# Kernel tuning notes

Measured on AMD Instinct MI355X. Metric: run time of the kernel, lower is better.

The kernel has to match this reference:

```python
import jax, jax.numpy as jnp
import numpy as np

# Model hyperparameters (from init_kwargs)
D_MODEL, D_STATE, D_CONV, EXPAND, NHEADS, NGROUPS = 1024, 16, 4, 2, 8, 1
D_INNER = D_MODEL * EXPAND                      # 2048
HEADDIM = D_INNER // NHEADS                     # 256
D_XBC = D_INNER + 2 * NGROUPS * D_STATE         # conv channels: x + B + C
D_IN_PROJ = 3 * D_INNER + D_XBC + NHEADS        # z0 + x0 + z(unused) + xBC + dt
BATCH, SEQLEN = 2, 2048
LN_EPS = 1e-5


def setup_inputs() -> dict:
    key = jax.random.key(0)
    ks = jax.random.split(key, 8)
    u = jax.random.normal(ks[0], (BATCH, SEQLEN, D_MODEL), dtype=jnp.float32)
    W_in = jax.random.normal(ks[1], (D_IN_PROJ, D_MODEL), jnp.float32) / np.sqrt(D_MODEL)
    conv_w = jax.random.normal(ks[2], (D_XBC, 1, D_CONV), jnp.float32) / np.sqrt(D_CONV)
    conv_b = jnp.zeros((D_XBC,), jnp.float32)
    # dt_bias = inverse-softplus of dt ~ LogUniform(1e-3, 1e-1), as in source init
    dt = jnp.exp(jax.random.uniform(ks[3], (NHEADS,)) * (np.log(0.1) - np.log(0.001)) + np.log(0.001))
    dt_bias = dt + jnp.log(-jnp.expm1(-dt))
    A_log = jnp.log(jax.random.uniform(ks[4], (NHEADS,), minval=0.9, maxval=0.999))
    D_param = jnp.ones((NHEADS,), jnp.float32)
    ln_gamma = jnp.ones((D_INNER,), jnp.float32)
    ln_beta = jnp.zeros((D_INNER,), jnp.float32)
    W_gate = jax.random.normal(ks[5], (D_INNER, D_INNER), jnp.float32) / np.sqrt(D_INNER)
    b_gate = jnp.zeros((D_INNER,), jnp.float32)
    W_out = jax.random.normal(ks[6], (D_MODEL, 2 * D_INNER), jnp.float32) / np.sqrt(2 * D_INNER)
    return dict(u=u, W_in=W_in, conv_w=conv_w, conv_b=conv_b, dt_bias=dt_bias,
                A_log=A_log, D_param=D_param, ln_gamma=ln_gamma, ln_beta=ln_beta,
                W_gate=W_gate, b_gate=b_gate, W_out=W_out)


def _silu(x):
    return x * jax.nn.sigmoid(x)


def reference(u, W_in, conv_w, conv_b, dt_bias, A_log, D_param,
              ln_gamma, ln_beta, W_gate, b_gate, W_out):
    B, L, _ = u.shape
    zxbcdt = u @ W_in.T                                   # [B,L,D_IN_PROJ]
    z0 = zxbcdt[..., :D_INNER]
    x0 = zxbcdt[..., D_INNER:2 * D_INNER]
    # z = zxbcdt[..., 2*D_INNER:3*D_INNER]  # split but never used in source forward
    xBC = zxbcdt[..., 3 * D_INNER:3 * D_INNER + D_XBC]
    dt = jax.nn.softplus(zxbcdt[..., -NHEADS:] + dt_bias)  # [B,L,H]
    A = -jnp.exp(A_log)                                    # [H], per-head scalar

    # causal depthwise conv1d over time (left pad d_conv-1, crop to L)
    xBC_c = jnp.transpose(xBC, (0, 2, 1))                  # [B,C,L]
    xBC_c = jax.lax.conv_general_dilated(
        xBC_c, conv_w, window_strides=(1,), padding=[(D_CONV - 1, 0)],
        dimension_numbers=('NCH', 'OIH', 'NCH'), feature_group_count=D_XBC)
    xBC = _silu(jnp.transpose(xBC_c, (0, 2, 1)) + conv_b)  # [B,L,C]

    x = xBC[..., :D_INNER].reshape(B, L, NHEADS, HEADDIM)  # [B,L,H,P]
    Bm = xBC[..., D_INNER:D_INNER + D_STATE]               # [B,L,N] (ngroups=1)
    Cm = xBC[..., D_INNER + D_STATE:]                      # [B,L,N]

    def step(h, inp):
        x_t, B_t, C_t, dt_t = inp                          # [B,H,P],[B,N],[B,N],[B,H]
        dA = jnp.exp(dt_t * A)[:, :, None, None]           # [B,H,1,1]
        h = dA * h + (dt_t[:, :, None, None] * x_t[..., None]) * B_t[:, None, None, :]
        y_t = jnp.einsum('bhpn,bn->bhp', h, C_t) + D_param[None, :, None] * x_t
        return h, y_t

    h0 = jnp.zeros((B, NHEADS, HEADDIM, D_STATE), u.dtype)
    xs = (jnp.moveaxis(x, 1, 0), jnp.moveaxis(Bm, 1, 0),
          jnp.moveaxis(Cm, 1, 0), jnp.moveaxis(dt, 1, 0))
    _, y = jax.lax.scan(step, h0, xs)                      # [L,B,H,P]
    y = jnp.moveaxis(y, 0, 1).reshape(B, L, D_INNER)

    # LayerNorm
    mu = y.mean(-1, keepdims=True)
    var = ((y - mu) ** 2).mean(-1, keepdims=True)
    y = (y - mu) * jax.lax.rsqrt(var + LN_EPS) * ln_gamma + ln_beta

    gate = jax.nn.sigmoid(y @ W_gate.T + b_gate)
    y = gate * y

    mlp_skip = _silu(z0) * x0
    return jnp.concatenate([mlp_skip, y], axis=-1) @ W_out.T  # [B,L,D_MODEL]
```

## Files before the change

### kernel.cpp

```cpp
#include <hip/hip_runtime.h>
#include <hip/hip_bf16.h>
#include <math.h>

#define BATCH   2
#define SEQLEN  2048
#define DMODEL  1024
#define DINNER  2048
#define DSTATE  16
#define NHEADS  8
#define HEADDIM 256
#define DXBC    2080
#define NPACK   6184
#define NPAD    6400
#define MROWS   4096
#define CHUNK   64
#define NCHUNK  32
#define BH      16

typedef unsigned int u32;
typedef unsigned short u16;
typedef __attribute__((ext_vector_type(8))) short short8;
typedef __attribute__((ext_vector_type(4))) float f32x4;

#define GLOAD16(g, l) __builtin_amdgcn_global_load_lds( \
    (const __attribute__((address_space(1))) u32*)(g),  \
    (__attribute__((address_space(3))) u32*)(l), 16, 0, 0)

#define MFMA_B16(d, a, b) d = __builtin_amdgcn_mfma_f32_16x16x32_bf16(a, b, d, 0, 0, 0)

__device__ __forceinline__ u16 f2bf(float f) {
  union { float f; u32 u; } v; v.f = f;
  u32 r = v.u + 0x7fff + ((v.u >> 16) & 1);
  return (u16)(r >> 16);
}
__device__ __forceinline__ float bf2f(u16 b) {
  union { u32 u; float f; } v; v.u = ((u32)b) << 16;
  return v.f;
}

struct GParts { float* p0; float* p1; };

#define S_U   1048576
#define S_WG  1048576
#define S_WO  1048576
#define S_WP  1638400
#define S_TOT (S_U + S_WG + S_WO + S_WP)

__global__ void cvt_all(const float* __restrict__ u, const float* __restrict__ Wg,
                        const float* __restrict__ Wo, const float* __restrict__ Win,
                        u16* __restrict__ ub, u16* __restrict__ Wgb,
                        u16* __restrict__ Wob, u16* __restrict__ Wp) {
  for (int i = blockIdx.x * 256 + threadIdx.x; i < S_TOT; i += gridDim.x * 256) {
    const float* src; u16* dst; int idx;
    if (i < S_U) { src = u; dst = ub; idx = i; }
    else if (i < S_U + S_WG) { src = Wg; dst = Wgb; idx = i - S_U; }
    else if (i < S_U + S_WG + S_WO) { src = Wo; dst = Wob; idx = i - S_U - S_WG; }
    else {
      int j = i - S_U - S_WG - S_WO;
      int row = j >> 8, c4 = j & 255;
      ushort4 o = make_ushort4(0, 0, 0, 0);
      if (row < NPACK) {
        int orig = row < 4096 ? row : row + 2048;
        float4 v = ((const float4*)(Win + (size_t)orig * DMODEL))[c4];
        o = make_ushort4(f2bf(v.x), f2bf(v.y), f2bf(v.z), f2bf(v.w));
      }
      ((ushort4*)Wp)[j] = o;
      continue;
    }
    float4 v = ((const float4*)src)[idx];
    ((ushort4*)dst)[idx] = make_ushort4(f2bf(v.x), f2bf(v.y), f2bf(v.z), f2bf(v.w));
  }
}

template <int NL>
__device__ __forceinline__ void stage_rows(const u16* __restrict__ gsrc, int ldk,
                                           char* ldsmat, int row0, int w, int l) {
  const int rl = w * 8 + (l >> 3);
  const int q = ((l & 7) ^ (l >> 3)) * 8;
  #pragma unroll
  for (int j = 0; j < NL; ++j) {
    GLOAD16(gsrc + (size_t)(row0 + j * 64 + rl) * ldk + q,
            ldsmat + (row0 + j * 64 + w * 8) * 128);
  }
}

__device__ __forceinline__ short8 frag8(const char* mat, int row, int q) {
  return *(const short8*)(mat + row * 128 + ((q ^ (row & 7)) << 4));
}

__global__ __launch_bounds__(512, 1) void gemmA(
    const u16* __restrict__ A, const u16* __restrict__ B, int K, int ldk,
    int ldo, u16* __restrict__ outp) {
  __shared__ char lds[131072];
  const int tid = threadIdx.x;
  const int w = tid >> 6, l = tid & 63;
  const int wm = w >> 2, wn = w & 3;
  const int fr = l & 15, g = l >> 4;
  int s = blockIdx.y * gridDim.x + blockIdx.x;
  const int nwg = gridDim.x * gridDim.y;
  s = (s & 7) * (nwg >> 3) + (s >> 3);
  const int bx = s % gridDim.x, by = s / gridDim.x;
  const u16* Ap = A + (size_t)bx * 256 * ldk;
  const u16* Bp = B + (size_t)by * 256 * ldk;
  const int NT = K >> 6;

  f32x4 acc[8][4];
  #pragma unroll
  for (int m = 0; m < 8; ++m)
    #pragma unroll
    for (int n = 0; n < 4; ++n) acc[m][n] = (f32x4){0.f, 0.f, 0.f, 0.f};

  stage_rows<2>(Bp, ldk, lds + 32768, 0, w, l);
  stage_rows<2>(Bp, ldk, lds + 32768, 128, w, l);
  stage_rows<1>(Ap, ldk, lds, 0, w, l);
  stage_rows<1>(Ap, ldk, lds, 128, w, l);
  stage_rows<1>(Ap, ldk, lds, 64, w, l);
  stage_rows<1>(Ap, ldk, lds, 192, w, l);

  for (int t = 0; t < NT; ++t) {
    const bool last = (t == NT - 1);
    const char* cbA = lds + (t & 1) * 65536;
    const char* cbB = cbA + 32768;
    char* nbA = lds + ((t + 1) & 1) * 65536;
    char* nbB = nbA + 32768;
    const u16* An = Ap + (size_t)(t + 1) * 64;
    const u16* Bn = Bp + (size_t)(t + 1) * 64;

    asm volatile("s_waitcnt vmcnt(2)" ::: "memory");
    __builtin_amdgcn_s_barrier();
    __builtin_amdgcn_sched_barrier(0);

    short8 bf0[4], bf1[4];
    #pragma unroll
    for (int n = 0; n < 4; ++n) {
      bf0[n] = frag8(cbB, wn * 64 + n * 16 + fr, g);
      bf1[n] = frag8(cbB, wn * 64 + n * 16 + fr, 4 + g);
    }
    {
      short8 a00 = frag8(cbA, wm * 128 + fr, g);
      short8 a01 = frag8(cbA, wm * 128 + fr, 4 + g);
      short8 a10 = frag8(cbA, wm * 128 + 16 + fr, g);
      short8 a11 = frag8(cbA, wm * 128 + 16 + fr, 4 + g);
      if (!last) stage_rows<2>(Bn, ldk, nbB, 0, w, l);
      asm volatile("s_waitcnt lgkmcnt(0)" ::: "memory");
      __builtin_amdgcn_sched_barrier(0);
      __builtin_amdgcn_s_setprio(1);
      #pragma unroll
      for (int n = 0; n < 4; ++n) { MFMA_B16(acc[0][n], a00, bf0[n]); MFMA_B16(acc[1][n], a10, bf0[n]); }
      #pragma unroll
      for (int n = 0; n < 4; ++n) { MFMA_B16(acc[0][n], a01, bf1[n]); MFMA_B16(acc[1][n], a11, bf1[n]); }
      __builtin_amdgcn_s_setprio(0);
    }
    {
      short8 a00 = frag8(cbA, wm * 128 + 32 + fr, g);
      short8 a01 = frag8(cbA, wm * 128 + 32 + fr, 4 + g);
      short8 a10 = frag8(cbA, wm * 128 + 48 + fr, g);
      short8 a11 = frag8(cbA, wm * 128 + 48 + fr, 4 + g);
      if (!last) stage_rows<2>(Bn, ldk, nbB, 128, w, l);
      asm volatile("s_waitcnt lgkmcnt(0)" ::: "memory");
      __builtin_amdgcn_sched_barrier(0);
      __builtin_amdgcn_s_setprio(1);
      #pragma unroll
      for (int n = 0; n < 4; ++n) { MFMA_B16(acc[2][n], a00, bf0[n]); MFMA_B16(acc[3][n], a10, bf0[n]); }
      #pragma unroll
      for (int n = 0; n < 4; ++n) { MFMA_B16(acc[2][n], a01, bf1[n]); MFMA_B16(acc[3][n], a11, bf1[n]); }
      __builtin_amdgcn_s_setprio(0);
    }
    if (last) { asm volatile("s_waitcnt vmcnt(0)" ::: "memory"); }
    else      { asm volatile("s_waitcnt vmcnt(4)" ::: "memory"); }
    __builtin_amdgcn_s_barrier();
    __builtin_amdgcn_sched_barrier(0);
    {
      short8 a00 = frag8(cbA, wm * 128 + 64 + fr, g);
      short8 a01 = frag8(cbA, wm * 128 + 64 + fr, 4 + g);
      short8 a10 = frag8(cbA, wm * 128 + 80 + fr, g);
      short8 a11 = frag8(cbA, wm * 128 + 80 + fr, 4 + g);
      if (!last) { stage_rows<1>(An, ldk, nbA, 0, w, l); stage_rows<1>(An, ldk, nbA, 128, w, l); }
      asm volatile("s_waitcnt lgkmcnt(0)" ::: "memory");
      __builtin_amdgcn_sched_barrier(0);
      __builtin_amdgcn_s_setprio(1);
      #pragma unroll
      for (int n = 0; n < 4; ++n) { MFMA_B16(acc[4][n], a00, bf0[n]); MFMA_B16(acc[5][n], a10, bf0[n]); }
      #pragma unroll
      for (int n = 0; n < 4; ++n) { MFMA_B16(acc[4][n], a01, bf1[n]); MFMA_B16(acc[5][n], a11, bf1[n]); }
      __builtin_amdgcn_s_setprio(0);
    }
    {
      short8 a00 = frag8(cbA, wm * 128 + 96 + fr, g);
      short8 a01 = frag8(cbA, wm * 128 + 96 + fr, 4 + g);
      short8 a10 = frag8(cbA, wm * 128 + 112 + fr, g);
      short8 a11 = frag8(cbA, wm * 128 + 112 + fr, 4 + g);
      if (!last) { stage_rows<1>(An, ldk, nbA, 64, w, l); stage_rows<1>(An, ldk, nbA, 192, w, l); }
      asm volatile("s_waitcnt lgkmcnt(0)" ::: "memory");
      __builtin_amdgcn_sched_barrier(0);
      __builtin_amdgcn_s_setprio(1);
      #pragma unroll
      for (int n = 0; n < 4; ++n) { MFMA_B16(acc[6][n], a00, bf0[n]); MFMA_B16(acc[7][n], a10, bf0[n]); }
      #pragma unroll
      for (int n = 0; n < 4; ++n) { MFMA_B16(acc[6][n], a01, bf1[n]); MFMA_B16(acc[7][n], a11, bf1[n]); }
      __builtin_amdgcn_s_setprio(0);
    }
  }

  const int er = g * 4;
  #pragma unroll
  for (int m = 0; m < 8; ++m)
    #pragma unroll
    for (int n = 0; n < 4; ++n)
      #pragma unroll
      for (int j = 0; j < 4; ++j) {
        int row = bx * 256 + wm * 128 + m * 16 + er + j;
        int col = by * 256 + wn * 64 + n * 16 + fr;
        outp[(size_t)row * ldo + col] = f2bf(acc[m][n][j]);
      }
}

template <int EPI>
__global__ __launch_bounds__(512, 1) void gemmB(
    const u16* __restrict__ A, const u16* __restrict__ B, int K_loop, int ldk,
    int ldo, void* __restrict__ outp, const float* __restrict__ bias,
    const u16* __restrict__ gate_in, GParts gp) {
  __shared__ char lds[3 * 49152];
  const int tid = threadIdx.x;
  const int w = tid >> 6, l = tid & 63;
  const int wm = w >> 1, wn = w & 1;
  const int fr = l & 15, g = l >> 4;
  int s = blockIdx.y * gridDim.x + blockIdx.x;
  const int nwg = gridDim.x * gridDim.y;
  s = (s & 7) * (nwg >> 3) + (s >> 3);
  const int bx = s % gridDim.x, by = s / gridDim.x;
  const u16* Ap = A + (size_t)bx * 256 * ldk + (size_t)blockIdx.z * K_loop;
  const u16* Bp = B + (size_t)by * 128 * ldk + (size_t)blockIdx.z * K_loop;
  const int NT = K_loop >> 6;

  f32x4 acc[4][4];
  #pragma unroll
  for (int m = 0; m < 4; ++m)
    #pragma unroll
    for (int n = 0; n < 4; ++n) acc[m][n] = (f32x4){0.f, 0.f, 0.f, 0.f};

  #pragma unroll
  for (int p = 0; p < 2; ++p) {
    char* bA = lds + p * 49152;
    char* bB = bA + 32768;
    const u16* Ak = Ap + (size_t)p * 64;
    const u16* Bk = Bp + (size_t)p * 64;
    stage_rows<1>(Bk, ldk, bB, 0, w, l);
    stage_rows<1>(Bk, ldk, bB, 64, w, l);
    stage_rows<1>(Ak, ldk, bA, 0, w, l);
    stage_rows<1>(Ak, ldk, bA, 64, w, l);
    stage_rows<1>(Ak, ldk, bA, 128, w, l);
    stage_rows<1>(Ak, ldk, bA, 192, w, l);
  }

  int cur = 0;
  for (int t = 0; t < NT; ++t) {
    const bool last = (t == NT - 1);
    const bool dostage = (t + 2 < NT);
    int st = cur + 2; if (st >= 3) st -= 3;
    const char* cbA = lds + cur * 49152;
    const char* cbB = cbA + 32768;
    char* nbA = lds + st * 49152;
    char* nbB = nbA + 32768;
    const u16* An = Ap + (size_t)(t + 2) * 64;
    const u16* Bn = Bp + (size_t)(t + 2) * 64;

    if (last) { asm volatile("s_waitcnt vmcnt(0)" ::: "memory"); }
    else      { asm volatile("s_waitcnt vmcnt(6)" ::: "memory"); }
    __builtin_amdgcn_s_barrier();
    __builtin_amdgcn_sched_barrier(0);

    short8 bf0[4], bf1[4];
    #pragma unroll
    for (int n = 0; n < 4; ++n) {
      bf0[n] = frag8(cbB, wn * 64 + n * 16 + fr, g);
      bf1[n] = frag8(cbB, wn * 64 + n * 16 + fr, 4 + g);
    }
    {
      short8 a00 = frag8(cbA, wm * 64 + fr, g);
      short8 a01 = frag8(cbA, wm * 64 + fr, 4 + g);
      short8 a10 = frag8(cbA, wm * 64 + 16 + fr, g);
      short8 a11 = frag8(cbA, wm * 64 + 16 + fr, 4 + g);
      if (dostage) {
        stage_rows<1>(Bn, ldk, nbB, 0, w, l);
        stage_rows<1>(Bn, ldk, nbB, 64, w, l);
        stage_rows<1>(An, ldk, nbA, 0, w, l);
      }
      asm volatile("s_waitcnt lgkmcnt(0)" ::: "memory");
      __builtin_amdgcn_sched_barrier(0);
      __builtin_amdgcn_s_setprio(1);
      #pragma unroll
      for (int n = 0; n < 4; ++n) { MFMA_B16(acc[0][n], a00, bf0[n]); MFMA_B16(acc[1][n], a10, bf0[n]); }
      #pragma unroll
      for (int n = 0; n < 4; ++n) { MFMA_B16(acc[0][n], a01, bf1[n]); MFMA_B16(acc[1][n], a11, bf1[n]); }
      __builtin_amdgcn_s_setprio(0);
    }
    {
      short8 a00 = frag8(cbA, wm * 64 + 32 + fr, g);
      short8 a01 = frag8(cbA, wm * 64 + 32 + fr, 4 + g);
      short8 a10 = frag8(cbA, wm * 64 + 48 + fr, g);
      short8 a11 = frag8(cbA, wm * 64 + 48 + fr, 4 + g);
      if (dostage) {
        stage_rows<1>(An, ldk, nbA, 64, w, l);
        stage_rows<1>(An, ldk, nbA, 128, w, l);
        stage_rows<1>(An, ldk, nbA, 192, w, l);
      }
      asm volatile("s_waitcnt lgkmcnt(0)" ::: "memory");
      __builtin_amdgcn_sched_barrier(0);
      __builtin_amdgcn_s_setprio(1);
      #pragma unroll
      for (int n = 0; n < 4; ++n) { MFMA_B16(acc[2][n], a00, bf0[n]); MFMA_B16(acc[3][n], a10, bf0[n]); }
      #pragma unroll
      for (int n = 0; n < 4; ++n) { MFMA_B16(acc[2][n], a01, bf1[n]); MFMA_B16(acc[3][n], a11, bf1[n]); }
      __builtin_amdgcn_s_setprio(0);
    }
    cur = cur + 1; if (cur >= 3) cur = 0;
  }

  const int er = g * 4;
  float* pp = nullptr;
  if (EPI == 2) pp = blockIdx.z == 0 ? gp.p0 : gp.p1;
  #pragma unroll
  for (int m = 0; m < 4; ++m)
    #pragma unroll
    for (int n = 0; n < 4; ++n)
      #pragma unroll
      for (int j = 0; j < 4; ++j) {
        int row = bx * 256 + wm * 64 + m * 16 + er + j;
        int col = by * 128 + wn * 64 + n * 16 + fr;
        float v = acc[m][n][j];
        if (EPI == 1) {
          float gt = 1.f / (1.f + __expf(-(v + bias[col])));
          float nv = bf2f(gate_in[(size_t)row * 2048 + col]);
          ((u16*)outp)[(size_t)row * 4096 + 2048 + col] = f2bf(gt * nv);
        } else {
          pp[(size_t)row * ldo + col] = v;
        }
      }
}

__global__ void reduce2(const float* __restrict__ p0, const float* __restrict__ p1,
                        float* __restrict__ out) {
  const int n4 = MROWS * DMODEL / 4;
  for (int i = blockIdx.x * 256 + threadIdx.x; i < n4; i += gridDim.x * 256) {
    float4 a = ((const float4*)p0)[i];
    float4 b = ((const float4*)p1)[i];
    float4 o;
    o.x = a.x + b.x; o.y = a.y + b.y; o.z = a.z + b.z; o.w = a.w + b.w;
    ((float4*)out)[i] = o;
  }
}

#define NB_CONV 33280
#define NB_MLP  8192
#define NB_DT   128

__global__ void prep_kernel(const u16* __restrict__ zx, const float* __restrict__ cw,
                            const float* __restrict__ cb, u16* __restrict__ xc,
                            float* __restrict__ bc, u16* __restrict__ hcat,
                            const float* __restrict__ dt_bias, float* __restrict__ dtb) {
  int blk = blockIdx.x;
  if (blk < NB_CONV) {
    int idx = blk * 256 + threadIdx.x;
    if (idx >= MROWS * DXBC) return;
    int c = idx % DXBC;
    int m = idx / DXBC;
    int l = m & (SEQLEN - 1);
    float acc = cb[c];
    float w0 = cw[c * 4 + 0], w1 = cw[c * 4 + 1], w2 = cw[c * 4 + 2], w3 = cw[c * 4 + 3];
    const u16* col = zx + (size_t)m * NPAD + 4096 + c;
    acc += w3 * bf2f(col[0]);
    if (l >= 1) acc += w2 * bf2f(col[-NPAD]);
    if (l >= 2) acc += w1 * bf2f(col[-2 * NPAD]);
    if (l >= 3) acc += w0 * bf2f(col[-3 * NPAD]);
    float sv = acc / (1.f + __expf(-acc));
    if (c < DINNER) xc[(size_t)m * DINNER + c] = f2bf(sv);
    else bc[(size_t)m * 32 + (c - DINNER)] = sv;
  } else if (blk < NB_CONV + NB_MLP) {
    int i = (blk - NB_CONV) * 256 + threadIdx.x;
    int m = i >> 9, c4 = (i & 511) * 4;
    const u16* row = zx + (size_t)m * NPAD;
    ushort4 zv = *(const ushort4*)(row + c4);
    ushort4 xv = *(const ushort4*)(row + 2048 + c4);
    float z0, x0;
    ushort4 o;
    z0 = bf2f(zv.x); x0 = bf2f(xv.x); o.x = f2bf(x0 * z0 / (1.f + __expf(-z0)));
    z0 = bf2f(zv.y); x0 = bf2f(xv.y); o.y = f2bf(x0 * z0 / (1.f + __expf(-z0)));
    z0 = bf2f(zv.z); x0 = bf2f(xv.z); o.z = f2bf(x0 * z0 / (1.f + __expf(-z0)));
    z0 = bf2f(zv.w); x0 = bf2f(xv.w); o.w = f2bf(x0 * z0 / (1.f + __expf(-z0)));
    *(ushort4*)(hcat + (size_t)m * 4096 + c4) = o;
  } else {
    int idx = (blk - NB_CONV - NB_MLP) * 256 + threadIdx.x;
    if (idx >= MROWS * NHEADS) return;
    int hd = idx & 7, m = idx >> 3;
    float raw = bf2f(zx[(size_t)m * NPAD + 6176 + hd]) + dt_bias[hd];
    float dtv = raw > 20.f ? raw : log1pf(expf(raw));
    dtb[idx] = dtv;
  }
}

__device__ __forceinline__ int xs_addr(int r, int p) {
  return r * 512 + ((((p >> 3) ^ ((r >> 3) & 3)) & 31) << 4) + (p & 7) * 2;
}
__device__ __forceinline__ int P_addr(int t, int s) {
  return t * 128 + ((((s >> 3) ^ (t & 7)) & 7) << 4) + (s & 7) * 2;
}

__device__ __forceinline__ void stage_x(u16* xs, const u16* __restrict__ xc,
                                        size_t base, int tid) {
  #pragma unroll
  for (int it = 0; it < 8; ++it) {
    int r = it * 8 + (tid >> 5);
    int pc = (tid & 31) * 8;
    short8 v = *(const short8*)(xc + base + (size_t)r * DINNER + pc);
    *(short8*)((char*)xs + xs_addr(r, pc)) = v;
  }
}

__device__ __forceinline__ short8 xfrag(const u16* xs, int k0, int g, int p) {
  short8 v;
  #pragma unroll
  for (int j = 0; j < 8; ++j) {
    int s = k0 + g * 8 + j;
    v[j] = *(const short*)((const char*)xs + xs_addr(s, p));
  }
  return v;
}

__global__ __launch_bounds__(256) void ssd_state(
    const u16* __restrict__ xc, const float* __restrict__ bcb,
    const float* __restrict__ dtb, const float* __restrict__ A_log,
    float* __restrict__ Sbuf, float* __restrict__ lcbuf) {
  __shared__ u16 xs[64 * 256];
  __shared__ float sLC[64], sDT[64];
  __shared__ float wBT[16][65];
  const int tid = threadIdx.x;
  const int bh = blockIdx.x >> 5, c = blockIdx.x & 31;
  const int b = bh >> 3, h = bh & 7;
  const size_t row0 = (size_t)b * SEQLEN + c * CHUNK;
  stage_x(xs, xc, row0 * DINNER + h * HEADDIM, tid);
  if (tid < 64) {
    float dtv = dtb[(row0 + tid) * NHEADS + h];
    float A = -__expf(A_log[h]);
    float s = dtv * A;
    #pragma unroll
    for (int off = 1; off < 64; off <<= 1) {
      float v = __shfl_up(s, off, 64);
      if (tid >= off) s += v;
    }
    sLC[tid] = s; sDT[tid] = dtv;
    lcbuf[(size_t)blockIdx.x * 64 + tid] = s;
  }
  __syncthreads();
  const float lc63 = sLC[63];
  for (int i = tid; i < 1024; i += 256) {
    int n = i & 15, t = i >> 4;
    float w = sDT[t] * __expf(lc63 - sLC[t]);
    wBT[n][t] = w * bcb[(row0 + t) * 32 + n];
  }
  __syncthreads();
  const int lane = tid & 63, w = tid >> 6;
  const int cl = lane & 15, g = lane >> 4;
  f32x4 acc[4];
  #pragma unroll
  for (int pt = 0; pt < 4; ++pt) acc[pt] = (f32x4){0.f, 0.f, 0.f, 0.f};
  #pragma unroll
  for (int kk = 0; kk < 2; ++kk) {
    int k0 = kk * 32;
    short8 af;
    #pragma unroll
    for (int j = 0; j < 8; ++j) af[j] = (short)f2bf(wBT[cl][k0 + g * 8 + j]);
    #pragma unroll
    for (int pt = 0; pt < 4; ++pt) {
      short8 bf = xfrag(xs, k0, g, (w * 4 + pt) * 16 + cl);
      acc[pt] = __builtin_amdgcn_mfma_f32_16x16x32_bf16(af, bf, acc[pt], 0, 0, 0);
    }
  }
  float* Sc = Sbuf + (size_t)blockIdx.x * 16 * 256;
  #pragma unroll
  for (int pt = 0; pt < 4; ++pt)
    #pragma unroll
    for (int j = 0; j < 4; ++j)
      Sc[(g * 4 + j) * 256 + (w * 4 + pt) * 16 + cl] = acc[pt][j];
}

__global__ __launch_bounds__(256) void ssd_combine(
    const float* __restrict__ Sbuf, const float* __restrict__ lcbuf,
    float* __restrict__ Sprev) {
  const int bh = blockIdx.x >> 4, seg = blockIdx.x & 15;
  const int idx = seg * 256 + threadIdx.x;
  float r = 0.f;
  #pragma unroll 1
  for (int c = 0; c < NCHUNK; ++c) {
    size_t o = ((size_t)bh * NCHUNK + c) * 4096 + idx;
    Sprev[o] = r;
    float lam = __expf(lcbuf[((size_t)bh * NCHUNK + c) * 64 + 63]);
    r = lam * r + Sbuf[o];
  }
}

__global__ __launch_bounds__(256) void ssd_out(
    const u16* __restrict__ xc, const float* __restrict__ bcb,
    const float* __restrict__ dtb, const float* __restrict__ lcbuf,
    const float* __restrict__ Sprev, const float* __restrict__ D_par,
    u16* __restrict__ y) {
  __shared__ u16 xs[64 * 256];
  __shared__ u16 P[64 * 64];
  __shared__ u16 sB[64][17], sC[64][17], sCe[64][17];
  __shared__ u16 sSp[256][17];
  __shared__ float sLC[64], sDT[64];
  const int tid = threadIdx.x;
  const int bh = blockIdx.x >> 5, c = blockIdx.x & 31;
  const int b = bh >> 3, h = bh & 7;
  const size_t row0 = (size_t)b * SEQLEN + c * CHUNK;
  stage_x(xs, xc, row0 * DINNER + h * HEADDIM, tid);
  if (tid < 64) {
    sLC[tid] = lcbuf[(size_t)blockIdx.x * 64 + tid];
    sDT[tid] = dtb[(row0 + tid) * NHEADS + h];
  }
  for (int i = tid; i < 1024; i += 256) {
    int n = i & 15, t = i >> 4;
    float Bv = bcb[(row0 + t) * 32 + n];
    float Cv = bcb[(row0 + t) * 32 + 16 + n];
    float e = __expf(lcbuf[(size_t)blockIdx.x * 64 + t]);
    sB[t][n] = f2bf(Bv);
    sC[t][n] = f2bf(Cv);
    sCe[t][n] = f2bf(Cv * e);
  }
  {
    const float* Sp = Sprev + (size_t)blockIdx.x * 4096;
    int p = tid & 255;
    if (tid < 256) {
      #pragma unroll
      for (int n = 0; n < 16; ++n) sSp[p][n] = f2bf(Sp[n * 256 + p]);
    }
  }
  __syncthreads();

  const int lane = tid & 63, w = tid >> 6;
  const int cl = lane & 15, g = lane >> 4;

  f32x4 gacc[4];
  #pragma unroll
  for (int st = 0; st < 4; ++st) gacc[st] = (f32x4){0.f, 0.f, 0.f, 0.f};
  short8 afc = (short8){0, 0, 0, 0, 0, 0, 0, 0};
  if (g < 2) {
    #pragma unroll
    for (int j = 0; j < 8; ++j) afc[j] = (short)sC[w * 16 + cl][g * 8 + j];
  }
  #pragma unroll
  for (int st = 0; st < 4; ++st) {
    short8 bfb = (short8){0, 0, 0, 0, 0, 0, 0, 0};
    if (g < 2) {
      #pragma unroll
      for (int j = 0; j < 8; ++j) bfb[j] = (short)sB[st * 16 + cl][g * 8 + j];
    }
    gacc[st] = __builtin_amdgcn_mfma_f32_16x16x32_bf16(afc, bfb, gacc[st], 0, 0, 0);
  }
  #pragma unroll
  for (int st = 0; st < 4; ++st) {
    #pragma unroll
    for (int j = 0; j < 4; ++j) {
      int t = w * 16 + g * 4 + j;
      int s = st * 16 + cl;
      float v = 0.f;
      if (s <= t) v = gacc[st][j] * sDT[s] * __expf(sLC[t] - sLC[s]);
      *(u16*)((char*)P + P_addr(t, s)) = f2bf(v);
    }
  }
  asm volatile("s_waitcnt lgkmcnt(0)" ::: "memory");
  __builtin_amdgcn_sched_barrier(0);

  f32x4 acc[16];
  #pragma unroll
  for (int pt = 0; pt < 16; ++pt) acc[pt] = (f32x4){0.f, 0.f, 0.f, 0.f};
  #pragma unroll
  for (int kk = 0; kk < 2; ++kk) {
    int k0 = kk * 32;
    short8 ap = *(const short8*)((const char*)P + P_addr(w * 16 + cl, k0 + g * 8));
    #pragma unroll
    for (int pt = 0; pt < 16; ++pt) {
      short8 bf = xfrag(xs, k0, g, pt * 16 + cl);
      acc[pt] = __builtin_amdgcn_mfma_f32_16x16x32_bf16(ap, bf, acc[pt], 0, 0, 0);
    }
  }
  {
    short8 ae = (short8){0, 0, 0, 0, 0, 0, 0, 0};
    if (g < 2) {
      #pragma unroll
      for (int j = 0; j < 8; ++j) ae[j] = (short)sCe[w * 16 + cl][g * 8 + j];
    }
    #pragma unroll
    for (int pt = 0; pt < 16; ++pt) {
      short8 bs = (short8){0, 0, 0, 0, 0, 0, 0, 0};
      if (g < 2) {
        #pragma unroll
        for (int j = 0; j < 8; ++j) bs[j] = (short)sSp[pt * 16 + cl][g * 8 + j];
      }
      acc[pt] = __builtin_amdgcn_mfma_f32_16x16x32_bf16(ae, bs, acc[pt], 0, 0, 0);
    }
  }
  const float Dv = D_par[h];
  #pragma unroll
  for (int pt = 0; pt < 16; ++pt) {
    #pragma unroll
    for (int j = 0; j < 4; ++j) {
      int t = w * 16 + g * 4 + j;
      int p = pt * 16 + cl;
      float xv = bf2f(*(const u16*)((const char*)xs + xs_addr(t, p)));
      float v = acc[pt][j] + Dv * xv;
      y[(row0 + t) * DINNER + h * HEADDIM + p] = f2bf(v);
    }
  }
}

__global__ __launch_bounds__(256) void ln_kernel(const u16* __restrict__ y,
                                                 const float* __restrict__ gamma,
                                                 const float* __restrict__ beta,
                                                 u16* __restrict__ nrm) {
  const int row = blockIdx.x;
  const int t = threadIdx.x;
  const u16* yr = y + (size_t)row * DINNER;
  short8 v = *(const short8*)(yr + t * 8);
  float f[8];
  float s = 0.f, ss = 0.f;
  #pragma unroll
  for (int j = 0; j < 8; ++j) {
    f[j] = bf2f((u16)v[j]);
    s += f[j]; ss += f[j] * f[j];
  }
  #pragma unroll
  for (int o = 1; o < 64; o <<= 1) { s += __shfl_xor(s, o); ss += __shfl_xor(ss, o); }
  __shared__ float rs[4], rss[4];
  const int wid = t >> 6;
  if ((t & 63) == 0) { rs[wid] = s; rss[wid] = ss; }
  __syncthreads();
  s = rs[0] + rs[1] + rs[2] + rs[3];
  ss = rss[0] + rss[1] + rss[2] + rss[3];
  float mu = s * (1.f / DINNER);
  float var = ss * (1.f / DINNER) - mu * mu;
  float inv = rsqrtf(var + 1e-5f);
  float4 g0 = ((const float4*)gamma)[t * 2], g1 = ((const float4*)gamma)[t * 2 + 1];
  float4 b0 = ((const float4*)beta)[t * 2], b1 = ((const float4*)beta)[t * 2 + 1];
  short8 o;
  o[0] = (short)f2bf((f[0] - mu) * inv * g0.x + b0.x);
  o[1] = (short)f2bf((f[1] - mu) * inv * g0.y + b0.y);
  o[2] = (short)f2bf((f[2] - mu) * inv * g0.z + b0.z);
  o[3] = (short)f2bf((f[3] - mu) * inv * g0.w + b0.w);
  o[4] = (short)f2bf((f[4] - mu) * inv * g1.x + b1.x);
  o[5] = (short)f2bf((f[5] - mu) * inv * g1.y + b1.y);
  o[6] = (short)f2bf((f[6] - mu) * inv * g1.z + b1.z);
  o[7] = (short)f2bf((f[7] - mu) * inv * g1.w + b1.w);
  *(short8*)(nrm + (size_t)row * DINNER + t * 8) = o;
}

extern "C" void kernel_launch(void* const* d_in, const int* in_sizes, int n_in,
                              void* d_out, int out_size, void* d_ws, size_t ws_size,
                              hipStream_t stream) {
  (void)in_sizes; (void)n_in; (void)out_size; (void)ws_size;
  const float* u       = (const float*)d_in[0];
  const float* W_in    = (const float*)d_in[1];
  const float* conv_w  = (const float*)d_in[2];
  const float* conv_b  = (const float*)d_in[3];
  const float* dt_bias = (const float*)d_in[4];
  const float* A_log   = (const float*)d_in[5];
  const float* D_par   = (const float*)d_in[6];
  const float* ln_g    = (const float*)d_in[7];
  const float* ln_b    = (const float*)d_in[8];
  const float* W_gate  = (const float*)d_in[9];
  const float* b_gate  = (const float*)d_in[10];
  const float* W_out   = (const float*)d_in[11];
  float* out = (float*)d_out;

  size_t off = 0;
  auto take = [&](size_t bytes) -> char* {
    char* p = (char*)d_ws + off;
    off = (off + bytes + 255) & ~(size_t)255;
    return p;
  };
  u16* u16b  = (u16*)take((size_t)MROWS * DMODEL * 2);
  u16* Wp    = (u16*)take((size_t)NPAD * DMODEL * 2);
  u16* Wg    = (u16*)take((size_t)DINNER * DINNER * 2);
  u16* Wo    = (u16*)take((size_t)DMODEL * 2 * DINNER * 2);
  u16* zx    = (u16*)take((size_t)MROWS * NPAD * 2);
  u16* xc    = (u16*)take((size_t)MROWS * DINNER * 2);
  float* bcb = (float*)take((size_t)MROWS * 32 * 4);
  float* dtb = (float*)take((size_t)MROWS * NHEADS * 4);
  float* lcbuf = (float*)take((size_t)BH * NCHUNK * 64 * 4);
  u16* nrm   = (u16*)take((size_t)MROWS * DINNER * 2);
  u16* hcat  = (u16*)take((size_t)MROWS * 2 * DINNER * 2);

  float* Sbuf  = (float*)u16b;
  u16*   y     = zx;
  float* Sprev = (float*)((char*)zx + (size_t)16 * 1024 * 1024);
  GParts parts2;
  parts2.p0 = (float*)zx;
  parts2.p1 = (float*)((char*)zx + (size_t)16 * 1024 * 1024);
  GParts none = {nullptr, nullptr};

  cvt_all<<<4096, 256, 0, stream>>>(u, W_gate, W_out, W_in, u16b, Wg, Wo, Wp);

  gemmA<<<dim3(MROWS / 256, NPAD / 256), 512, 0, stream>>>(
      u16b, Wp, DMODEL, DMODEL, NPAD, zx);

  prep_kernel<<<NB_CONV + NB_MLP + NB_DT, 256, 0, stream>>>(
      zx, conv_w, conv_b, xc, bcb, hcat, dt_bias, dtb);

  ssd_state<<<BH * NCHUNK, 256, 0, stream>>>(xc, bcb, dtb, A_log, Sbuf, lcbuf);
  ssd_combine<<<BH * 16, 256, 0, stream>>>(Sbuf, lcbuf, Sprev);
  ssd_out<<<BH * NCHUNK, 256, 0, stream>>>(xc, bcb, dtb, lcbuf, Sprev, D_par, y);

  ln_kernel<<<MROWS, 256, 0, stream>>>(y, ln_g, ln_b, nrm);

  gemmB<1><<<dim3(MROWS / 256, DINNER / 128), 512, 0, stream>>>(
      nrm, Wg, DINNER, DINNER, 0, hcat, b_gate, nrm, none);

  gemmB<2><<<dim3(MROWS / 256, DMODEL / 128, 2), 512, 0, stream>>>(
      hcat, Wo, 2 * DINNER / 2, 2 * DINNER, DMODEL, nullptr, nullptr, nullptr, parts2);

  reduce2<<<2048, 256, 0, stream>>>(parts2.p0, parts2.p1, out);
}
```

Before: 252.7 us.

## Fold split-K reduction into atomics, vectorize conv prep, drop explicit LDS waits

The second split-K output GEMM now atomically adds its fp32 partials straight into a zeroed output buffer. This replaces the two partial buffers and the separate reduce2 kernel with a memset plus atomics. The depthwise conv in the prep kernel handles two channels per thread with vectorized loads and stores, which halves its block count. The explicit lgkmcnt(0) waits before the MFMA groups in both GEMMs are removed, leaving LDS wait placement to the compiler. The cost is atomic traffic and contention at L2, plus results that depend on the order of the two adds.

```diff
diff --git a/kernel.cpp b/kernel.cpp
--- a/kernel.cpp
+++ b/kernel.cpp
@@ -37,8 +37,6 @@
   union { u32 u; float f; } v; v.u = ((u32)b) << 16;
   return v.f;
 }
-
-struct GParts { float* p0; float* p1; };
 
 #define S_U   1048576
 #define S_WG  1048576
@@ -142,7 +140,6 @@
       short8 a10 = frag8(cbA, wm * 128 + 16 + fr, g);
       short8 a11 = frag8(cbA, wm * 128 + 16 + fr, 4 + g);
       if (!last) stage_rows<2>(Bn, ldk, nbB, 0, w, l);
-      asm volatile("s_waitcnt lgkmcnt(0)" ::: "memory");
       __builtin_amdgcn_sched_barrier(0);
       __builtin_amdgcn_s_setprio(1);
       #pragma unroll
@@ -157,7 +154,6 @@
       short8 a10 = frag8(cbA, wm * 128 + 48 + fr, g);
       short8 a11 = frag8(cbA, wm * 128 + 48 + fr, 4 + g);
       if (!last) stage_rows<2>(Bn, ldk, nbB, 128, w, l);
-      asm volatile("s_waitcnt lgkmcnt(0)" ::: "memory");
       __builtin_amdgcn_sched_barrier(0);
       __builtin_amdgcn_s_setprio(1);
       #pragma unroll
@@ -176,7 +172,6 @@
       short8 a10 = frag8(cbA, wm * 128 + 80 + fr, g);
       short8 a11 = frag8(cbA, wm * 128 + 80 + fr, 4 + g);
       if (!last) { stage_rows<1>(An, ldk, nbA, 0, w, l); stage_rows<1>(An, ldk, nbA, 128, w, l); }
-      asm volatile("s_waitcnt lgkmcnt(0)" ::: "memory");
       __builtin_amdgcn_sched_barrier(0);
       __builtin_amdgcn_s_setprio(1);
       #pragma unroll
@@ -191,7 +186,6 @@
       short8 a10 = frag8(cbA, wm * 128 + 112 + fr, g);
       short8 a11 = frag8(cbA, wm * 128 + 112 + fr, 4 + g);
       if (!last) { stage_rows<1>(An, ldk, nbA, 64, w, l); stage_rows<1>(An, ldk, nbA, 192, w, l); }
-      asm volatile("s_waitcnt lgkmcnt(0)" ::: "memory");
       __builtin_amdgcn_sched_barrier(0);
       __builtin_amdgcn_s_setprio(1);
       #pragma unroll
@@ -219,7 +213,7 @@
 __global__ __launch_bounds__(512, 1) void gemmB(
     const u16* __restrict__ A, const u16* __restrict__ B, int K_loop, int ldk,
     int ldo, void* __restrict__ outp, const float* __restrict__ bias,
-    const u16* __restrict__ gate_in, GParts gp) {
+    const u16* __restrict__ gate_in) {
   __shared__ char lds[3 * 49152];
   const int tid = threadIdx.x;
   const int w = tid >> 6, l = tid & 63;
@@ -286,7 +280,6 @@
         stage_rows<1>(Bn, ldk, nbB, 64, w, l);
         stage_rows<1>(An, ldk, nbA, 0, w, l);
       }
-      asm volatile("s_waitcnt lgkmcnt(0)" ::: "memory");
       __builtin_amdgcn_sched_barrier(0);
       __builtin_amdgcn_s_setprio(1);
       #pragma unroll
@@ -305,7 +298,6 @@
         stage_rows<1>(An, ldk, nbA, 128, w, l);
         stage_rows<1>(An, ldk, nbA, 192, w, l);
       }
-      asm volatile("s_waitcnt lgkmcnt(0)" ::: "memory");
       __builtin_amdgcn_sched_barrier(0);
       __builtin_amdgcn_s_setprio(1);
       #pragma unroll
@@ -318,8 +310,6 @@
   }
 
   const int er = g * 4;
-  float* pp = nullptr;
-  if (EPI == 2) pp = blockIdx.z == 0 ? gp.p0 : gp.p1;
   #pragma unroll
   for (int m = 0; m < 4; ++m)
     #pragma unroll
@@ -334,24 +324,12 @@
           float nv = bf2f(gate_in[(size_t)row * 2048 + col]);
           ((u16*)outp)[(size_t)row * 4096 + 2048 + col] = f2bf(gt * nv);
         } else {
-          pp[(size_t)row * ldo + col] = v;
+          atomicAdd(&((float*)outp)[(size_t)row * ldo + col], v);
         }
       }
 }
 
-__global__ void reduce2(const float* __restrict__ p0, const float* __restrict__ p1,
-                        float* __restrict__ out) {
-  const int n4 = MROWS * DMODEL / 4;
-  for (int i = blockIdx.x * 256 + threadIdx.x; i < n4; i += gridDim.x * 256) {
-    float4 a = ((const float4*)p0)[i];
-    float4 b = ((const float4*)p1)[i];
-    float4 o;
-    o.x = a.x + b.x; o.y = a.y + b.y; o.z = a.z + b.z; o.w = a.w + b.w;
-    ((float4*)out)[i] = o;
-  }
-}
-
-#define NB_CONV 33280
+#define NB_CONV 16640
 #define NB_MLP  8192
 #define NB_DT   128
 
@@ -362,20 +340,29 @@
   int blk = blockIdx.x;
   if (blk < NB_CONV) {
     int idx = blk * 256 + threadIdx.x;
-    if (idx >= MROWS * DXBC) return;
-    int c = idx % DXBC;
-    int m = idx / DXBC;
+    int c2 = idx % (DXBC / 2);
+    int m = idx / (DXBC / 2);
+    int c = c2 * 2;
     int l = m & (SEQLEN - 1);
-    float acc = cb[c];
-    float w0 = cw[c * 4 + 0], w1 = cw[c * 4 + 1], w2 = cw[c * 4 + 2], w3 = cw[c * 4 + 3];
     const u16* col = zx + (size_t)m * NPAD + 4096 + c;
-    acc += w3 * bf2f(col[0]);
-    if (l >= 1) acc += w2 * bf2f(col[-NPAD]);
-    if (l >= 2) acc += w1 * bf2f(col[-2 * NPAD]);
-    if (l >= 3) acc += w0 * bf2f(col[-3 * NPAD]);
-    float sv = acc / (1.f + __expf(-acc));
-    if (c < DINNER) xc[(size_t)m * DINNER + c] = f2bf(sv);
-    else bc[(size_t)m * 32 + (c - DINNER)] = sv;
+    float2 cbv = *(const float2*)(cb + c);
+    float4 w0 = ((const float4*)cw)[c2 * 2];
+    float4 w1 = ((const float4*)cw)[c2 * 2 + 1];
+    float a0 = cbv.x, a1 = cbv.y;
+    ushort2 t0 = *(const ushort2*)col;
+    a0 += w0.w * bf2f(t0.x); a1 += w1.w * bf2f(t0.y);
+    if (l >= 1) { ushort2 t = *(const ushort2*)(col - NPAD);     a0 += w0.z * bf2f(t.x); a1 += w1.z * bf2f(t.y); }
+    if (l >= 2) { ushort2 t = *(const ushort2*)(col - 2 * NPAD); a0 += w0.y * bf2f(t.x); a1 += w1.y * bf2f(t.y); }
+    if (l >= 3) { ushort2 t = *(const ushort2*)(col - 3 * NPAD); a0 += w0.x * bf2f(t.x); a1 += w1.x * bf2f(t.y); }
+    float s0 = a0 / (1.f + __expf(-a0));
+    float s1 = a1 / (1.f + __expf(-a1));
+    if (c < DINNER) {
+      ushort2 o; o.x = f2bf(s0); o.y = f2bf(s1);
+      *(ushort2*)(xc + (size_t)m * DINNER + c) = o;
+    } else {
+      float2 o; o.x = s0; o.y = s1;
+      *(float2*)(bc + (size_t)m * 32 + (c - DINNER)) = o;
+    }
   } else if (blk < NB_CONV + NB_MLP) {
     int i = (blk - NB_CONV) * 256 + threadIdx.x;
     int m = i >> 9, c4 = (i & 511) * 4;
@@ -693,10 +680,6 @@
   float* Sbuf  = (float*)u16b;
   u16*   y     = zx;
   float* Sprev = (float*)((char*)zx + (size_t)16 * 1024 * 1024);
-  GParts parts2;
-  parts2.p0 = (float*)zx;
-  parts2.p1 = (float*)((char*)zx + (size_t)16 * 1024 * 1024);
-  GParts none = {nullptr, nullptr};
 
   cvt_all<<<4096, 256, 0, stream>>>(u, W_gate, W_out, W_in, u16b, Wg, Wo, Wp);
 
@@ -713,10 +696,9 @@
   ln_kernel<<<MROWS, 256, 0, stream>>>(y, ln_g, ln_b, nrm);
 
   gemmB<1><<<dim3(MROWS / 256, DINNER / 128), 512, 0, stream>>>(
-      nrm, Wg, DINNER, DINNER, 0, hcat, b_gate, nrm, none);
-
+      nrm, Wg, DINNER, DINNER, 0, hcat, b_gate, nrm);
+
+  hipMemsetAsync(out, 0, (size_t)MROWS * DMODEL * 4, stream);
   gemmB<2><<<dim3(MROWS / 256, DMODEL / 128, 2), 512, 0, stream>>>(
-      hcat, Wo, 2 * DINNER / 2, 2 * DINNER, DMODEL, nullptr, nullptr, nullptr, parts2);
-
-  reduce2<<<2048, 256, 0, stream>>>(parts2.p0, parts2.p1, out);
-}
+      hcat, Wo, 2 * DINNER / 2, 2 * DINNER, DMODEL, out, nullptr, nullptr);
+}
```

Measured after the change: 263.9 us. 4.4% more time.
